# Kernel optimization log

Hardware: AMD Instinct MI355X
Metric: run time of the kernel (lower is better)

The kernel has to match this reference:

```python
import jax, jax.numpy as jnp
import numpy as np

B = 16384
ED = 32          # embed_dim
NF = 16          # num_filters
KS = [1, 3, 5, 7, 9]
LENS = {"pep": 12, "a1": 7, "a2": 8, "a3": 22, "b1": 6, "b2": 7, "b3": 23}


def setup_inputs() -> dict:
    key = jax.random.key(0)
    keys = jax.random.split(key, 32)
    ki = iter(keys)
    inp = {}
    for name, L in LENS.items():
        inp[name] = jax.random.normal(next(ki), (B, ED, L), dtype=jnp.float32)
    # conv weights: one stack of 7 convs per kernel size; w{k}: [7, NF, ED, k], bias c{k}: [7, NF]
    for k in KS:
        fan_in = ED * k
        bound = 1.0 / np.sqrt(fan_in)
        inp[f"w{k}"] = jax.random.uniform(next(ki), (7, NF, ED, k), jnp.float32, -bound, bound)
        inp[f"c{k}"] = jax.random.uniform(next(ki), (7, NF), jnp.float32, -bound, bound)
    dbound = 1.0 / np.sqrt(NF * 35)
    inp["dw"] = jax.random.uniform(next(ki), (NF * 35, 1), jnp.float32, -dbound, dbound)
    inp["db"] = jax.random.uniform(next(ki), (1,), jnp.float32, -dbound, dbound)
    return inp


def _branch(x, w, b):
    # x: [B, ED, L], w: [NF, ED, k], b: [NF] -> [B, NF] (conv 'same' + relu + global max)
    y = jax.lax.conv_general_dilated(x, w, window_strides=(1,), padding="SAME",
                                     dimension_numbers=("NCH", "OIH", "NCH"))
    y = jax.nn.relu(y + b[None, :, None])
    return jnp.max(y, axis=2)


def reference(pep, a1, a2, a3, b1, b2, b3, w1, w3, w5, w7, w9, c1, c3, c5, c7, c9, dw, db):
    xs = [pep, a1, a2, a3, b1, b2, b3]
    ws = {1: w1, 3: w3, 5: w5, 7: w7, 9: w9}
    cs = {1: c1, 3: c3, 5: c5, 7: c7, 9: c9}
    feats = []
    for i, x in enumerate(xs):  # fixed 7 inputs
        for k in KS:            # fixed 5 kernel sizes
            feats.append(_branch(x, ws[k][i], cs[k][i]))
    feat = jnp.concatenate(feats, axis=1)        # [B, 35*NF]
    out = jax.nn.sigmoid(feat @ dw + db)         # [B, 1]
    return jnp.squeeze(out, axis=-1)             # [B]
```

## Files before the change

### kernel.cpp

```cpp
#include <hip/hip_runtime.h>
#include <cmath>

namespace {

using bf16x8 = __attribute__((ext_vector_type(8))) short;
using f32x4  = __attribute__((ext_vector_type(4))) float;

constexpr int NT = 192;
constexpr int NS = 16;
constexpr int TILE_BYTES = NS * 31 * 32 * 2;
constexpr int B = 16384;
constexpr int NTILE = B / NS;

__device__ __forceinline__ short f2bf(float f) {
  unsigned u = __float_as_uint(f);
  return (short)((u + 0x7FFFu + ((u >> 16) & 1u)) >> 16);
}

__device__ __forceinline__ int gidx(int s, int q, int cq) {
  return (s * 31 + q) * 4 + ((cq ^ ((s >> 1) + (q >> 1))) & 3);
}

__device__ __forceinline__ bf16x8 ldcol(const char* smem, int s, int cq, int q) {
  return *(const bf16x8*)(smem + (gidx(s, q, cq) << 4));
}

template<int K1, int K2>
__device__ __forceinline__ void run_role(
    const char* __restrict__ smem, int s, int cq, int f,
    const float* __restrict__ wk1, const float* __restrict__ ck1,
    const float* __restrict__ wk2, const float* __restrict__ ck2,
    const float* __restrict__ dw, int i, int L, f32x4& dvec)
{
  constexpr int KK1 = (K1 - 1) / 2;
  constexpr int KK2 = (K2 > 0) ? (K2 - 1) / 2 : 0;

  bf16x8 wf1[K1];
  #pragma unroll
  for (int t = 0; t < K1; ++t) {
    const float* wp = wk1 + (size_t)((i * 16 + f) * 32 + cq * 8) * K1 + t;
    bf16x8 v;
    #pragma unroll
    for (int j = 0; j < 8; ++j) v[j] = f2bf(wp[(size_t)j * K1]);
    wf1[t] = v;
  }
  bf16x8 wf2[(K2 > 0) ? K2 : 1];
  if constexpr (K2 > 0) {
    #pragma unroll
    for (int t = 0; t < K2; ++t) {
      const float* wp = wk2 + (size_t)((i * 16 + f) * 32 + cq * 8) * K2 + t;
      bf16x8 v;
      #pragma unroll
      for (int j = 0; j < 8; ++j) v[j] = f2bf(wp[(size_t)j * K2]);
      wf2[t] = v;
    }
  }

  const float b1 = ck1[i * 16 + f];
  float b2 = 0.f;
  if constexpr (K2 > 0) b2 = ck2[i * 16 + f];

  f32x4 mx1 = {0.f, 0.f, 0.f, 0.f};
  f32x4 mx2 = {0.f, 0.f, 0.f, 0.f};

  bf16x8 af[K1];
  #pragma unroll
  for (int j = 0; j < K1; ++j) af[j] = ldcol(smem, s, cq, 4 - KK1 + j);

  auto body = [&](int p, int pi) {
    f32x4 aa = {b1, b1, b1, b1};
    f32x4 ab = {0.f, 0.f, 0.f, 0.f};
    #pragma unroll
    for (int t = 0; t < K1; ++t) {
      if (t & 1)
        ab = __builtin_amdgcn_mfma_f32_16x16x32_bf16(af[(pi + t) % K1], wf1[t], ab, 0, 0, 0);
      else
        aa = __builtin_amdgcn_mfma_f32_16x16x32_bf16(af[(pi + t) % K1], wf1[t], aa, 0, 0, 0);
    }
    if constexpr (K2 > 0) {
      f32x4 ac = {b2, b2, b2, b2};
      #pragma unroll
      for (int t = 0; t < K2; ++t)
        ac = __builtin_amdgcn_mfma_f32_16x16x32_bf16(af[(pi + (KK1 - KK2) + t) % K1], wf2[t], ac, 0, 0, 0);
      #pragma unroll
      for (int r = 0; r < 4; ++r) mx2[r] = fmaxf(mx2[r], ac[r]);
    }
    #pragma unroll
    for (int r = 0; r < 4; ++r) mx1[r] = fmaxf(mx1[r], aa[r] + ab[r]);
    if (p + pi + 1 < L)
      af[pi] = ldcol(smem, s, cq, p + pi + 5 + KK1);
  };

  __builtin_amdgcn_s_setprio(1);
  int p = 0;
  for (; p + K1 <= L; p += K1) {
    #pragma unroll
    for (int pi = 0; pi < K1; ++pi) body(p, pi);
  }
  #pragma unroll
  for (int pi = 0; pi < K1 - 1; ++pi)
    if (p + pi < L) body(p, pi);
  __builtin_amdgcn_s_setprio(0);

  {
    const float dv1 = dw[(i * 5 + KK1) * 16 + f];
    #pragma unroll
    for (int r = 0; r < 4; ++r) dvec[r] = fmaf(mx1[r], dv1, dvec[r]);
  }
  if constexpr (K2 > 0) {
    const float dv2 = dw[(i * 5 + KK2) * 16 + f];
    #pragma unroll
    for (int r = 0; r < 4; ++r) dvec[r] = fmaf(mx2[r], dv2, dvec[r]);
  }
}

__global__ __launch_bounds__(NT, 2) void nettcr_mfma(
    const float* __restrict__ x0, const float* __restrict__ x1,
    const float* __restrict__ x2, const float* __restrict__ x3,
    const float* __restrict__ x4, const float* __restrict__ x5,
    const float* __restrict__ x6,
    const float* __restrict__ w1, const float* __restrict__ c1,
    const float* __restrict__ w3, const float* __restrict__ c3,
    const float* __restrict__ w5, const float* __restrict__ c5,
    const float* __restrict__ w7, const float* __restrict__ c7,
    const float* __restrict__ w9, const float* __restrict__ c9,
    const float* __restrict__ dw,
    float* __restrict__ part)
{
  __shared__ __align__(16) char smem[TILE_BYTES];
  const int tid  = threadIdx.x;
  const int lane = tid & 63;
  const int wid  = tid >> 6;
  const int bx   = blockIdx.x;
  const int i    = bx % 7;
  const int b0   = (bx / 7) * NS;
  const int s    = lane & 15;
  const int cq   = lane >> 4;
  const int f    = lane & 15;

  const float* xi; int L;
  switch (i) {
    case 0: xi = x0; L = 12; break;
    case 1: xi = x1; L = 7;  break;
    case 2: xi = x2; L = 8;  break;
    case 3: xi = x3; L = 22; break;
    case 4: xi = x4; L = 6;  break;
    case 5: xi = x5; L = 7;  break;
    default: xi = x6; L = 23; break;
  }

  for (int e = tid; e < 64 * L; e += NT) {
    const int l  = e % L;
    const int rr = e / L;
    const int cg = rr & 3;
    const int ss = rr >> 2;
    const float* src = xi + ((size_t)(b0 + ss) * 32 + cg * 8) * L + l;
    bf16x8 pk;
    #pragma unroll
    for (int jj = 0; jj < 8; ++jj) pk[jj] = f2bf(src[(size_t)jj * L]);
    *(bf16x8*)(smem + (gidx(ss, l + 4, cg) << 4)) = pk;
  }
  for (int e = tid; e < 512; e += NT) {
    const int q8 = e & 7;
    const int q  = (q8 < 4) ? q8 : (L + q8);
    const int cg = (e >> 3) & 3;
    const int ss = e >> 5;
    bf16x8 z = {0, 0, 0, 0, 0, 0, 0, 0};
    *(bf16x8*)(smem + (gidx(ss, q, cg) << 4)) = z;
  }
  __syncthreads();

  f32x4 dvec = {0.f, 0.f, 0.f, 0.f};
  if (wid == 0)
    run_role<9, 0>(smem, s, cq, f, w9, c9, nullptr, nullptr, dw, i, L, dvec);
  else if (wid == 1)
    run_role<7, 1>(smem, s, cq, f, w7, c7, w1, c1, dw, i, L, dvec);
  else
    run_role<5, 3>(smem, s, cq, f, w5, c5, w3, c3, dw, i, L, dvec);

  __syncthreads();
  float* red = (float*)smem;
  *(f32x4*)&red[(wid * 64 + lane) * 4] = dvec;
  __syncthreads();
  if (tid < 16) {
    float sum = 0.f;
    const int g4 = tid >> 2, r = tid & 3;
    for (int w = 0; w < 3; ++w)
      #pragma unroll
      for (int f2 = 0; f2 < 16; ++f2)
        sum += red[(w * 64 + g4 * 16 + f2) * 4 + r];
    part[i * B + b0 + tid] = sum;
  }
}

__global__ void combine_sigmoid(const float* __restrict__ part,
                                const float* __restrict__ db,
                                float* __restrict__ out)
{
  const int i = blockIdx.x * blockDim.x + threadIdx.x;
  if (i < B) {
    float sum = db[0];
    #pragma unroll
    for (int j = 0; j < 7; ++j) sum += part[j * B + i];
    out[i] = 1.0f / (1.0f + expf(-sum));
  }
}

}

extern "C" void kernel_launch(void* const* d_in, const int* in_sizes, int n_in,
                              void* d_out, int out_size, void* d_ws, size_t ws_size,
                              hipStream_t stream) {
  (void)ws_size; (void)out_size;
  const float* xs[7];
  for (int i = 0; i < 7; ++i) xs[i] = (const float*)d_in[i];

  const float* wptr[5] = {nullptr, nullptr, nullptr, nullptr, nullptr};
  const float* cptr[5] = {nullptr, nullptr, nullptr, nullptr, nullptr};
  const float* dw = nullptr;
  const float* db = nullptr;
  int c_seen = 0;
  for (int idx = 7; idx < n_in; ++idx) {
    const int sz = in_sizes[idx];
    const float* p = (const float*)d_in[idx];
    if (sz == 1) { db = p; }
    else if (sz == 16 * 35) { dw = p; }
    else if (sz == 7 * 16) { cptr[c_seen++] = p; }
    else {
      const int k = sz / (7 * 16 * 32);
      wptr[(k - 1) / 2] = p;
    }
  }

  float* part = (float*)d_ws;

  dim3 grid(7 * NTILE), block(NT);
  hipLaunchKernelGGL(nettcr_mfma, grid, block, 0, stream,
                     xs[0], xs[1], xs[2], xs[3], xs[4], xs[5], xs[6],
                     wptr[0], cptr[0], wptr[1], cptr[1], wptr[2], cptr[2],
                     wptr[3], cptr[3], wptr[4], cptr[4], dw, part);

  hipLaunchKernelGGL(combine_sigmoid, dim3((B + 255) / 256), dim3(256), 0, stream,
                     part, db, (float*)d_out);
}
```

Before: 113.2 us.

## Make blocks persistent over four tiles with register-staged double-buffered loads

Each block now handles four consecutive 16-sample tiles instead of one. The next tile's global loads are issued into registers before the current tile's MFMA compute, then converted to bf16 and written to a second LDS buffer, so load latency overlaps compute. Weights are converted once per block rather than once per tile, and the K1 accumulation is split across three chains for the larger kernels. This costs a double-sized LDS footprint, heavy register staging (64 floats per thread), dropping the 2-waves-per-EU launch bound, and a four-times smaller grid, all of which may reduce occupancy.

Result: slower. 135.6 us (+19.8%).

```diff
diff --git a/kernel.cpp b/kernel.cpp
--- a/kernel.cpp
+++ b/kernel.cpp
@@ -10,7 +10,8 @@
 constexpr int NS = 16;
 constexpr int TILE_BYTES = NS * 31 * 32 * 2;
 constexpr int B = 16384;
-constexpr int NTILE = B / NS;
+constexpr int T = 4;
+constexpr int ITEMS = 8;
 
 __device__ __forceinline__ short f2bf(float f) {
   unsigned u = __float_as_uint(f);
@@ -21,19 +22,129 @@
   return (s * 31 + q) * 4 + ((cq ^ ((s >> 1) + (q >> 1))) & 3);
 }
 
-__device__ __forceinline__ bf16x8 ldcol(const char* smem, int s, int cq, int q) {
-  return *(const bf16x8*)(smem + (gidx(s, q, cq) << 4));
+__device__ __forceinline__ bf16x8 ldcol(const char* buf, int s, int cq, int q) {
+  return *(const bf16x8*)(buf + (gidx(s, q, cq) << 4));
+}
+
+struct StageRegs {
+  float v[ITEMS][8];
+  int   off[ITEMS];
+};
+
+__device__ __forceinline__ void stage_issue(const float* __restrict__ xi, int L,
+                                            int b0, int tid, StageRegs& sr) {
+  int l  = tid % L;
+  int rr = tid / L;
+  const int qd = NT / L, rd = NT % L;
+  #pragma unroll
+  for (int u = 0; u < ITEMS; ++u) {
+    sr.off[u] = -1;
+    if (u * NT + tid < 64 * L) {
+      const int cg = rr & 3;
+      const int ss = rr >> 2;
+      const float* src = xi + ((size_t)(b0 + ss) * 32 + cg * 8) * L + l;
+      #pragma unroll
+      for (int j = 0; j < 8; ++j) sr.v[u][j] = src[(size_t)j * L];
+      sr.off[u] = gidx(ss, l + 4, cg) << 4;
+    }
+    l += rd; rr += qd;
+    if (l >= L) { l -= L; rr += 1; }
+  }
+}
+
+__device__ __forceinline__ void stage_write(char* __restrict__ buf, const StageRegs& sr) {
+  #pragma unroll
+  for (int u = 0; u < ITEMS; ++u) {
+    if (sr.off[u] >= 0) {
+      bf16x8 pk;
+      #pragma unroll
+      for (int j = 0; j < 8; ++j) pk[j] = f2bf(sr.v[u][j]);
+      *(bf16x8*)(buf + sr.off[u]) = pk;
+    }
+  }
 }
 
 template<int K1, int K2>
-__device__ __forceinline__ void run_role(
-    const char* __restrict__ smem, int s, int cq, int f,
-    const float* __restrict__ wk1, const float* __restrict__ ck1,
-    const float* __restrict__ wk2, const float* __restrict__ ck2,
-    const float* __restrict__ dw, int i, int L, f32x4& dvec)
+__device__ __forceinline__ f32x4 compute_tile(
+    const char* __restrict__ buf, int s, int cq, int L,
+    const bf16x8 (&wf1)[K1], const bf16x8 (&wf2)[(K2 > 0) ? K2 : 1],
+    float b1, float b2, float dv1, float dv2)
 {
   constexpr int KK1 = (K1 - 1) / 2;
   constexpr int KK2 = (K2 > 0) ? (K2 - 1) / 2 : 0;
+  constexpr int NCH = (K1 >= 7) ? 3 : 2;
+
+  f32x4 mx1 = {0.f, 0.f, 0.f, 0.f};
+  f32x4 mx2 = {0.f, 0.f, 0.f, 0.f};
+
+  bf16x8 af[K1];
+  #pragma unroll
+  for (int j = 0; j < K1; ++j) af[j] = ldcol(buf, s, cq, 4 - KK1 + j);
+
+  auto body = [&](int p, int pi) {
+    f32x4 ca = {b1, b1, b1, b1};
+    f32x4 cb = {0.f, 0.f, 0.f, 0.f};
+    f32x4 cc = {0.f, 0.f, 0.f, 0.f};
+    #pragma unroll
+    for (int t = 0; t < K1; ++t) {
+      const int m = t % NCH;
+      if (m == 0)
+        ca = __builtin_amdgcn_mfma_f32_16x16x32_bf16(af[(pi + t) % K1], wf1[t], ca, 0, 0, 0);
+      else if (m == 1)
+        cb = __builtin_amdgcn_mfma_f32_16x16x32_bf16(af[(pi + t) % K1], wf1[t], cb, 0, 0, 0);
+      else
+        cc = __builtin_amdgcn_mfma_f32_16x16x32_bf16(af[(pi + t) % K1], wf1[t], cc, 0, 0, 0);
+    }
+    if constexpr (K2 > 0) {
+      f32x4 cd = {b2, b2, b2, b2};
+      #pragma unroll
+      for (int t = 0; t < K2; ++t)
+        cd = __builtin_amdgcn_mfma_f32_16x16x32_bf16(af[(pi + (KK1 - KK2) + t) % K1], wf2[t], cd, 0, 0, 0);
+      #pragma unroll
+      for (int r = 0; r < 4; ++r) mx2[r] = fmaxf(mx2[r], cd[r]);
+    }
+    #pragma unroll
+    for (int r = 0; r < 4; ++r) {
+      float tot = ca[r] + cb[r];
+      if constexpr (NCH == 3) tot += cc[r];
+      mx1[r] = fmaxf(mx1[r], tot);
+    }
+    if (p + pi + 1 < L)
+      af[pi] = ldcol(buf, s, cq, p + pi + 5 + KK1);
+  };
+
+  __builtin_amdgcn_s_setprio(1);
+  int p = 0;
+  for (; p + K1 <= L; p += K1) {
+    #pragma unroll
+    for (int pi = 0; pi < K1; ++pi) body(p, pi);
+  }
+  #pragma unroll
+  for (int pi = 0; pi < K1 - 1; ++pi)
+    if (p + pi < L) body(p, pi);
+  __builtin_amdgcn_s_setprio(0);
+
+  f32x4 dv = {0.f, 0.f, 0.f, 0.f};
+  #pragma unroll
+  for (int r = 0; r < 4; ++r) {
+    dv[r] = mx1[r] * dv1;
+    if constexpr (K2 > 0) dv[r] = fmaf(mx2[r], dv2, dv[r]);
+  }
+  return dv;
+}
+
+template<int K1, int K2>
+__device__ __forceinline__ void role_main(
+    char* __restrict__ bufA, char* __restrict__ bufB,
+    float* __restrict__ redA, float* __restrict__ redB,
+    const float* __restrict__ xi, int L, int i, int tile0,
+    int tid, int s, int cq, int f,
+    const float* __restrict__ wk1, const float* __restrict__ ck1,
+    const float* __restrict__ wk2, const float* __restrict__ ck2,
+    const float* __restrict__ dw, float* __restrict__ part)
+{
+  constexpr int KK1 = (K1 - 1) / 2;
+  constexpr int KK2 = (K2 > 0) ? (K2 - 1) / 2 : 0;
 
   bf16x8 wf1[K1];
   #pragma unroll
@@ -55,66 +166,39 @@
       wf2[t] = v;
     }
   }
-
   const float b1 = ck1[i * 16 + f];
-  float b2 = 0.f;
-  if constexpr (K2 > 0) b2 = ck2[i * 16 + f];
-
-  f32x4 mx1 = {0.f, 0.f, 0.f, 0.f};
-  f32x4 mx2 = {0.f, 0.f, 0.f, 0.f};
-
-  bf16x8 af[K1];
-  #pragma unroll
-  for (int j = 0; j < K1; ++j) af[j] = ldcol(smem, s, cq, 4 - KK1 + j);
-
-  auto body = [&](int p, int pi) {
-    f32x4 aa = {b1, b1, b1, b1};
-    f32x4 ab = {0.f, 0.f, 0.f, 0.f};
-    #pragma unroll
-    for (int t = 0; t < K1; ++t) {
-      if (t & 1)
-        ab = __builtin_amdgcn_mfma_f32_16x16x32_bf16(af[(pi + t) % K1], wf1[t], ab, 0, 0, 0);
-      else
-        aa = __builtin_amdgcn_mfma_f32_16x16x32_bf16(af[(pi + t) % K1], wf1[t], aa, 0, 0, 0);
-    }
-    if constexpr (K2 > 0) {
-      f32x4 ac = {b2, b2, b2, b2};
-      #pragma unroll
-      for (int t = 0; t < K2; ++t)
-        ac = __builtin_amdgcn_mfma_f32_16x16x32_bf16(af[(pi + (KK1 - KK2) + t) % K1], wf2[t], ac, 0, 0, 0);
-      #pragma unroll
-      for (int r = 0; r < 4; ++r) mx2[r] = fmaxf(mx2[r], ac[r]);
-    }
-    #pragma unroll
-    for (int r = 0; r < 4; ++r) mx1[r] = fmaxf(mx1[r], aa[r] + ab[r]);
-    if (p + pi + 1 < L)
-      af[pi] = ldcol(smem, s, cq, p + pi + 5 + KK1);
-  };
-
-  __builtin_amdgcn_s_setprio(1);
-  int p = 0;
-  for (; p + K1 <= L; p += K1) {
-    #pragma unroll
-    for (int pi = 0; pi < K1; ++pi) body(p, pi);
-  }
-  #pragma unroll
-  for (int pi = 0; pi < K1 - 1; ++pi)
-    if (p + pi < L) body(p, pi);
-  __builtin_amdgcn_s_setprio(0);
-
-  {
-    const float dv1 = dw[(i * 5 + KK1) * 16 + f];
-    #pragma unroll
-    for (int r = 0; r < 4; ++r) dvec[r] = fmaf(mx1[r], dv1, dvec[r]);
-  }
-  if constexpr (K2 > 0) {
-    const float dv2 = dw[(i * 5 + KK2) * 16 + f];
-    #pragma unroll
-    for (int r = 0; r < 4; ++r) dvec[r] = fmaf(mx2[r], dv2, dvec[r]);
-  }
-}
-
-__global__ __launch_bounds__(NT, 2) void nettcr_mfma(
+  const float b2 = (K2 > 0) ? ck2[i * 16 + f] : 0.f;
+  const float dv1 = dw[(i * 5 + KK1) * 16 + f];
+  const float dv2 = (K2 > 0) ? dw[(i * 5 + KK2) * 16 + f] : 0.f;
+
+  StageRegs sr;
+  stage_issue(xi, L, tile0 * NS, tid, sr);
+  stage_write(bufA, sr);
+  __syncthreads();
+
+  char* cur = bufA; char* nxt = bufB;
+  float* rcur = redA; float* rnxt = redB;
+  for (int t = 0; t < T; ++t) {
+    if (t + 1 < T) stage_issue(xi, L, (tile0 + t + 1) * NS, tid, sr);
+    f32x4 dvec = compute_tile<K1, K2>(cur, s, cq, L, wf1, wf2, b1, b2, dv1, dv2);
+    *(f32x4*)&rcur[tid * 4] = dvec;
+    if (t + 1 < T) stage_write(nxt, sr);
+    __syncthreads();
+    if (tid < 16) {
+      float sum = 0.f;
+      const int g4 = tid >> 2, r = tid & 3;
+      for (int w = 0; w < 3; ++w)
+        #pragma unroll
+        for (int f2 = 0; f2 < 16; ++f2)
+          sum += rcur[(w * 64 + g4 * 16 + f2) * 4 + r];
+      part[i * B + (tile0 + t) * NS + tid] = sum;
+    }
+    { char* tb = cur; cur = nxt; nxt = tb; }
+    { float* tr = rcur; rcur = rnxt; rnxt = tr; }
+  }
+}
+
+__global__ __launch_bounds__(NT) void nettcr_mfma(
     const float* __restrict__ x0, const float* __restrict__ x1,
     const float* __restrict__ x2, const float* __restrict__ x3,
     const float* __restrict__ x4, const float* __restrict__ x5,
@@ -127,13 +211,17 @@
     const float* __restrict__ dw,
     float* __restrict__ part)
 {
-  __shared__ __align__(16) char smem[TILE_BYTES];
+  __shared__ __align__(16) char bufA[TILE_BYTES];
+  __shared__ __align__(16) char bufB[TILE_BYTES];
+  __shared__ float redA[NT * 4];
+  __shared__ float redB[NT * 4];
+
   const int tid  = threadIdx.x;
   const int lane = tid & 63;
   const int wid  = tid >> 6;
   const int bx   = blockIdx.x;
   const int i    = bx % 7;
-  const int b0   = (bx / 7) * NS;
+  const int tile0 = (bx / 7) * T;
   const int s    = lane & 15;
   const int cq   = lane >> 4;
   const int f    = lane & 15;
@@ -149,48 +237,28 @@
     default: xi = x6; L = 23; break;
   }
 
-  for (int e = tid; e < 64 * L; e += NT) {
-    const int l  = e % L;
-    const int rr = e / L;
-    const int cg = rr & 3;
-    const int ss = rr >> 2;
-    const float* src = xi + ((size_t)(b0 + ss) * 32 + cg * 8) * L + l;
-    bf16x8 pk;
-    #pragma unroll
-    for (int jj = 0; jj < 8; ++jj) pk[jj] = f2bf(src[(size_t)jj * L]);
-    *(bf16x8*)(smem + (gidx(ss, l + 4, cg) << 4)) = pk;
-  }
-  for (int e = tid; e < 512; e += NT) {
-    const int q8 = e & 7;
-    const int q  = (q8 < 4) ? q8 : (L + q8);
-    const int cg = (e >> 3) & 3;
-    const int ss = e >> 5;
-    bf16x8 z = {0, 0, 0, 0, 0, 0, 0, 0};
-    *(bf16x8*)(smem + (gidx(ss, q, cg) << 4)) = z;
-  }
-  __syncthreads();
-
-  f32x4 dvec = {0.f, 0.f, 0.f, 0.f};
+  {
+    const bf16x8 z = {0, 0, 0, 0, 0, 0, 0, 0};
+    for (int e = tid; e < 1024; e += NT) {
+      char* bb = (e & 512) ? bufB : bufA;
+      const int r  = e & 511;
+      const int q8 = r & 7;
+      const int q  = (q8 < 4) ? q8 : (L + q8);
+      const int cg = (r >> 3) & 3;
+      const int ss = r >> 5;
+      *(bf16x8*)(bb + (gidx(ss, q, cg) << 4)) = z;
+    }
+  }
+
   if (wid == 0)
-    run_role<9, 0>(smem, s, cq, f, w9, c9, nullptr, nullptr, dw, i, L, dvec);
+    role_main<9, 0>(bufA, bufB, redA, redB, xi, L, i, tile0, tid, s, cq, f,
+                    w9, c9, nullptr, nullptr, dw, part);
   else if (wid == 1)
-    run_role<7, 1>(smem, s, cq, f, w7, c7, w1, c1, dw, i, L, dvec);
+    role_main<7, 1>(bufA, bufB, redA, redB, xi, L, i, tile0, tid, s, cq, f,
+                    w7, c7, w1, c1, dw, part);
   else
-    run_role<5, 3>(smem, s, cq, f, w5, c5, w3, c3, dw, i, L, dvec);
-
-  __syncthreads();
-  float* red = (float*)smem;
-  *(f32x4*)&red[(wid * 64 + lane) * 4] = dvec;
-  __syncthreads();
-  if (tid < 16) {
-    float sum = 0.f;
-    const int g4 = tid >> 2, r = tid & 3;
-    for (int w = 0; w < 3; ++w)
-      #pragma unroll
-      for (int f2 = 0; f2 < 16; ++f2)
-        sum += red[(w * 64 + g4 * 16 + f2) * 4 + r];
-    part[i * B + b0 + tid] = sum;
-  }
+    role_main<5, 3>(bufA, bufB, redA, redB, xi, L, i, tile0, tid, s, cq, f,
+                    w5, c5, w3, c3, dw, part);
 }
 
 __global__ void combine_sigmoid(const float* __restrict__ part,
@@ -234,7 +302,7 @@
 
   float* part = (float*)d_ws;
 
-  dim3 grid(7 * NTILE), block(NT);
+  dim3 grid(7 * (B / NS / T)), block(NT);
   hipLaunchKernelGGL(nettcr_mfma, grid, block, 0, stream,
                      xs[0], xs[1], xs[2], xs[3], xs[4], xs[5], xs[6],
                      wptr[0], cptr[0], wptr[1], cptr[1], wptr[2], cptr[2],
```
